# Performance work log

Measured on AMD Instinct MI355X. Metric: run time of the kernel, lower is better.

Reference implementation:

```python
import jax, jax.numpy as jnp
import numpy as np

N, C_IN, HF, WF = 4, 256, 128, 128
IMG_H, IMG_W = 1024, 1024
A = 3  # anchors per location (1 size x 3 aspect ratios), matches RPNHead
OBJ_THR, IOU_THR = 0.3, 0.7
PRE_NMS, POST_NMS = 2000, 300  # pre-NMS top-k (== top_k_proposals_training), post-NMS top-k (testing)


def setup_inputs() -> dict:
    key = jax.random.key(0)
    ks = jax.random.split(key, 5)
    return {
        "feat": jax.random.normal(ks[0], (N, C_IN, HF, WF), jnp.float32),
        "conv_w": jax.random.normal(ks[1], (256, C_IN, 3, 3), jnp.float32) * 0.02,
        "conv_b": jnp.zeros((256,), jnp.float32),
        "det_w": jax.random.normal(ks[2], (A, 256, 1, 1), jnp.float32) * 0.05,
        "det_b": jnp.zeros((A,), jnp.float32),
        "reg_w": jax.random.normal(ks[3], (4 * A, 256, 1, 1), jnp.float32) * 0.02,
        "reg_b": jnp.zeros((4 * A,), jnp.float32),
    }


def _conv(x, w, b, pad):
    y = jax.lax.conv_general_dilated(x, w, (1, 1), [(pad, pad), (pad, pad)],
                                     dimension_numbers=("NCHW", "OIHW", "NCHW"))
    return y + b[None, :, None, None]


def _anchors():
    # AnchorGenerator.generate_anchors + grid_anchors, stride = image // grid
    scales = jnp.array([128.0], jnp.float32)
    ratios = jnp.array([0.5, 1.0, 2.0], jnp.float32)
    hr = jnp.sqrt(ratios)
    wr = 1.0 / hr
    ws = (wr[:, None] * scales[None, :]).reshape(-1)
    hs = (hr[:, None] * scales[None, :]).reshape(-1)
    base = jnp.round(jnp.stack([-ws, -hs, ws, hs], axis=1) / 2.0)  # [A,4]
    sx = jnp.arange(WF, dtype=jnp.float32) * (IMG_W // WF)
    sy = jnp.arange(HF, dtype=jnp.float32) * (IMG_H // HF)
    yy, xx = jnp.meshgrid(sy, sx, indexing="ij")
    shifts = jnp.stack([xx.ravel(), yy.ravel(), xx.ravel(), yy.ravel()], axis=1)  # [H*W,4]
    return (shifts[:, None, :] + base[None, :, :]).reshape(-1, 4)  # [H*W*A,4]


def _decode(anchors, deltas):
    # Faithful to source, including the x/y swap in the anchor-center computation.
    x1, y1, x2, y2 = anchors[..., 0], anchors[..., 1], anchors[..., 2], anchors[..., 3]
    aw = x2 - x1
    ah = y2 - y1
    acx = y1 + aw / 2  # (sic) matches original code
    acy = x1 + ah / 2  # (sic)
    dx, dy, dw, dh = deltas[..., 0], deltas[..., 1], deltas[..., 2], deltas[..., 3]
    px = acx + dx * aw
    py = acy + dy * ah
    pw = aw * jnp.exp(dw)
    ph = ah * jnp.exp(dh)
    return jnp.stack([px - pw / 2, py - ph / 2, px + pw / 2, py + ph / 2], axis=-1)


def _filter_one(boxes, scores):
    # clip -> degenerate filter -> objectness threshold -> NMS -> top-k, fixed shapes
    w = boxes[:, 2] - boxes[:, 0]
    h = boxes[:, 3] - boxes[:, 1]
    valid = (scores > OBJ_THR) & (w > 0) & (h > 0)
    s = jnp.where(valid, scores, -jnp.inf)
    top_s, top_i = jax.lax.top_k(s, PRE_NMS)
    b = boxes[top_i]
    v = valid[top_i]
    area = jnp.maximum(b[:, 2] - b[:, 0], 0) * jnp.maximum(b[:, 3] - b[:, 1], 0)
    ix1 = jnp.maximum(b[:, None, 0], b[None, :, 0])
    iy1 = jnp.maximum(b[:, None, 1], b[None, :, 1])
    ix2 = jnp.minimum(b[:, None, 2], b[None, :, 2])
    iy2 = jnp.minimum(b[:, None, 3], b[None, :, 3])
    inter = jnp.maximum(ix2 - ix1, 0) * jnp.maximum(iy2 - iy1, 0)
    iou = inter / jnp.maximum(area[:, None] + area[None, :] - inter, 1e-9)
    idxs = jnp.arange(PRE_NMS)

    def body(keep, i):
        sup = jnp.any((iou[i] > IOU_THR) & keep & (idxs < i))
        return keep.at[i].set(v[i] & ~sup), None

    keep, _ = jax.lax.scan(body, jnp.zeros(PRE_NMS, bool), idxs)
    fs = jnp.where(keep, top_s, -jnp.inf)
    sel_s, sel_i = jax.lax.top_k(fs, POST_NMS)
    kept = keep[sel_i]
    out = jnp.concatenate([b[sel_i], sel_s[:, None]], axis=-1)  # [POST,5] = box + score
    return jnp.where(kept[:, None], out, 0.0)


def reference(feat, conv_w, conv_b, det_w, det_b, reg_w, reg_b):
    x = _conv(feat, conv_w, conv_b, 1)                      # fpn conv 3x3, no activation
    obj = jax.nn.sigmoid(_conv(x, det_w, det_b, 0)).reshape(N, -1)  # [N, A*H*W]
    d = _conv(x, reg_w, reg_b, 0)                           # [N, 4A, H, W]
    d = d.reshape(N, 4, A, HF, WF).transpose(0, 2, 3, 4, 1).reshape(N, -1, 4)
    anchors = _anchors()                                    # [A_total, 4]
    props = _decode(anchors[None], d)
    props = jnp.stack([
        jnp.clip(props[..., 0], 0, IMG_W), jnp.clip(props[..., 1], 0, IMG_H),
        jnp.clip(props[..., 2], 0, IMG_W), jnp.clip(props[..., 3], 0, IMG_H)], axis=-1)
    return jax.vmap(_filter_one)(props, obj)  # [N, POST_NMS, 5]
```

## Files before the change

### kernel.cpp

```cpp
#include <hip/hip_runtime.h>
#include <hip/hip_bf16.h>
#include <hip/hip_fp16.h>
#include <stdint.h>
#include <math.h>

#define N_IMG 4
#define CIN 256
#define HFD 128
#define WFD 128
#define HW (HFD*WFD)
#define NA 3
#define NPROP (NA*HW)
#define PRE_NMS 2000
#define POST_NMS 300

__device__ __forceinline__ unsigned long long rl64(unsigned long long v, int i) {
    unsigned int lo = (unsigned int)__builtin_amdgcn_readlane((int)(unsigned int)v, i);
    unsigned int hi = (unsigned int)__builtin_amdgcn_readlane((int)(unsigned int)(v >> 32), i);
    return ((unsigned long long)hi << 32) | (unsigned long long)lo;
}

__device__ __forceinline__ double sum8(const double* __restrict__ PART, size_t cp) {
    const size_t S = (size_t)1 << 20;
    double a = PART[cp] + PART[cp + S];
    double b = PART[cp + 2 * S] + PART[cp + 3 * S];
    double c = PART[cp + 4 * S] + PART[cp + 5 * S];
    double d = PART[cp + 6 * S] + PART[cp + 7 * S];
    return (a + b) + (c + d);
}

__device__ __forceinline__ void decode_box(int i, double dx, double dy, double dwv, double dhv,
                                           double& c1o, double& c2o, double& c3o, double& c4o) {
    int loc = i / 3, aa = i % 3;
    int hh = loc >> 7, wwi = loc & 127;
    double sx = (double)(wwi * 8), sy = (double)(hh * 8);
    double bx1 = (aa == 0) ? -91.0 : (aa == 1 ? -64.0 : -45.0);
    double by1 = (aa == 0) ? -45.0 : (aa == 1 ? -64.0 : -91.0);
    double x1 = sx + bx1, y1 = sy + by1, x2 = sx - bx1, y2 = sy - by1;
    double aw = x2 - x1, ahh = y2 - y1;
    double acx = y1 + aw * 0.5;
    double acy = x1 + ahh * 0.5;
    double px = acx + dx * aw, py = acy + dy * ahh;
    double pw = aw * exp(dwv), ph = ahh * exp(dhv);
    double c1 = px - pw * 0.5, c2 = py - ph * 0.5, c3 = px + pw * 0.5, c4 = py + ph * 0.5;
    c1o = fmin(fmax(c1, 0.0), 1024.0);
    c2o = fmin(fmax(c2, 0.0), 1024.0);
    c3o = fmin(fmax(c3, 0.0), 1024.0);
    c4o = fmin(fmax(c4, 0.0), 1024.0);
}

__global__ __launch_bounds__(256) void k_effw64(const float* __restrict__ cw, const float* __restrict__ cb,
                                                const float* __restrict__ dw_, const float* __restrict__ db_,
                                                const float* __restrict__ rw_, const float* __restrict__ rb_,
                                                double* __restrict__ E64, double* __restrict__ EB64)
{
    int b = blockIdx.x;
    int tid = threadIdx.x;
    if (b < 144) {
        __shared__ float hwl[15][260];
        __shared__ float wt[256][16];
        int k0 = b * 16;
        for (int idx = tid; idx < 15 * 256; idx += 256) {
            int c = idx >> 8, co = idx & 255;
            hwl[c][co] = (c < 3) ? dw_[c * 256 + co] : rw_[(c - 3) * 256 + co];
        }
        for (int idx = tid; idx < 4096; idx += 256) {
            int co = idx >> 4, kk = idx & 15;
            wt[co][kk] = cw[co * 2304 + k0 + kk];
        }
        __syncthreads();
        int kk = tid >> 4, c = tid & 15;
        double s = 0.0;
        if (c < 15) {
#pragma unroll 4
            for (int co = 0; co < 256; co++) s += (double)hwl[c][co] * (double)wt[co][kk];
        }
        E64[(k0 + kk) * 16 + c] = s;
    } else {
        if (tid < 16) {
            int c = tid;
            double s = 0.0; double hb = 0.0;
            if (c < 15) {
                const float* hw = (c < 3) ? (dw_ + c * 256) : (rw_ + (c - 3) * 256);
                for (int co = 0; co < 256; co++) s += (double)hw[co] * (double)cb[co];
                hb = (double)((c < 3) ? db_[c] : rb_[c - 3]);
            }
            EB64[c] = s + hb;
        }
    }
}

__global__ __launch_bounds__(256, 4) void k_conv64(const float* __restrict__ feat,
                                                   const double* __restrict__ E64,
                                                   double* __restrict__ PART)
{
    __shared__ float in_t[8][6][132];
    __shared__ double wl[8][9][16];
    int b = blockIdx.x;
    int chunk = b & 7; int htile = (b >> 3) & 31; int n = b >> 8;
    int h0 = htile * 4;
    int tid = threadIdx.x;
    int q = tid & 63, hl = tid >> 6;
    int w0 = q * 2;
    double acc[15][2];
#pragma unroll
    for (int c = 0; c < 15; c++) { acc[c][0] = 0.0; acc[c][1] = 0.0; }

    for (int sl = 0; sl < 4; sl++) {
        int ci0 = (chunk << 5) + sl * 8;
        for (int idx = tid; idx < 8 * 780; idx += 256) {
            int ci = idx / 780; int r2 = idx % 780; int dh = r2 / 130; int dw = r2 % 130;
            int gh = h0 - 1 + dh, gw = dw - 1;
            float v = 0.f;
            if (gh >= 0 && gh < HFD && gw >= 0 && gw < WFD)
                v = feat[(((n << 8) + ci0 + ci) << 14) + (gh << 7) + gw];
            in_t[ci][dh][dw] = v;
        }
        for (int idx = tid; idx < 1152; idx += 256) {
            ((double*)wl)[idx] = E64[(size_t)ci0 * 144 + idx];
        }
        __syncthreads();
        for (int ci = 0; ci < 8; ci++) {
#pragma unroll
            for (int r = 0; r < 3; r++) {
                float2 g0 = *(const float2*)&in_t[ci][hl + r][w0];
                float2 g1 = *(const float2*)&in_t[ci][hl + r][w0 + 2];
                float f[4] = {g0.x, g0.y, g1.x, g1.y};
#pragma unroll
                for (int s = 0; s < 3; s++) {
                    const double* wp = &wl[ci][r * 3 + s][0];
                    double pa = (double)f[s], pb = (double)f[s + 1];
#pragma unroll
                    for (int cp = 0; cp < 7; cp++) {
                        double2 wv = *(const double2*)(wp + 2 * cp);
                        acc[2 * cp][0] += wv.x * pa; acc[2 * cp][1] += wv.x * pb;
                        acc[2 * cp + 1][0] += wv.y * pa; acc[2 * cp + 1][1] += wv.y * pb;
                    }
                    double w14 = wp[14];
                    acc[14][0] += w14 * pa; acc[14][1] += w14 * pb;
                }
            }
        }
        __syncthreads();
    }
    int gpos = (n << 14) + ((h0 + hl) << 7) + w0;
    double* base = PART + ((size_t)chunk << 20) + gpos;
#pragma unroll
    for (int c = 0; c < 15; c++) {
        double2 st; st.x = acc[c][0]; st.y = acc[c][1];
        *(double2*)(base + (size_t)c * 65536) = st;
    }
}

__global__ __launch_bounds__(256) void k_findecode(const double* __restrict__ PART,
                                                   const double* __restrict__ EB64,
                                                   unsigned long long* __restrict__ KEY64)
{
    int p = blockIdx.x * 256 + threadIdx.x;
    int n = p >> 14, pos = p & 16383;
    double L[15];
#pragma unroll
    for (int c = 0; c < 15; c++)
        L[c] = sum8(PART, (size_t)c * 65536 + p) + EB64[c];
#pragma unroll
    for (int a = 0; a < 3; a++) {
        double logit = L[a];
        double score = 1.0 / (1.0 + exp(-logit));
        int i = a * HW + pos;
        double c1, c2, c3, c4;
        decode_box(i, L[3 + a], L[6 + a], L[9 + a], L[12 + a], c1, c2, c3, c4);
        bool valid = (score > 0.3) && (c3 - c1 > 0.0) && (c4 - c2 > 0.0);
        KEY64[(size_t)n * NPROP + i] = valid ? ~((unsigned long long)__double_as_longlong(score)) : ~0ull;
    }
}

__global__ __launch_bounds__(256) void k_selinit(unsigned long long* __restrict__ PSPREF,
                                                 int* __restrict__ PSNEED,
                                                 uint32_t* __restrict__ HIST,
                                                 uint32_t* __restrict__ CNT)
{
    int idx = blockIdx.x * 256 + threadIdx.x;
    if (idx < N_IMG * 2048) HIST[idx] = 0u;
    if (idx < N_IMG) { PSPREF[idx] = 0ull; PSNEED[idx] = PRE_NMS; CNT[idx] = 0u; }
}

__global__ __launch_bounds__(256) void k_hist(const unsigned long long* __restrict__ KEY64,
                                              const unsigned long long* __restrict__ PSPREF,
                                              uint32_t* __restrict__ HIST, int L)
{
    __shared__ uint32_t h[2048];
    int blk = blockIdx.x; int n = blk >> 4, sub = blk & 15;
    int tid = threadIdx.x;
    for (int i = tid; i < 2048; i += 256) h[i] = 0u;
    __syncthreads();
    int sh = 53 - 11 * L;
    unsigned long long pref = PSPREF[n];
    const unsigned long long* K = KEY64 + (size_t)n * NPROP + sub * 3072;
    for (int i = tid; i < 3072; i += 256) {
        unsigned long long k = K[i];
        bool in = (L == 0) || ((k >> (sh + 11)) == pref);
        if (in) atomicAdd(&h[(uint32_t)((k >> sh) & 2047ull)], 1u);
    }
    __syncthreads();
    uint32_t* G = HIST + n * 2048;
    for (int i = tid; i < 2048; i += 256) {
        uint32_t v = h[i];
        if (v) atomicAdd(&G[i], v);
    }
}

__global__ __launch_bounds__(256) void k_pick(uint32_t* __restrict__ HIST,
                                              unsigned long long* __restrict__ PSPREF,
                                              int* __restrict__ PSNEED)
{
    int n = blockIdx.x; int tid = threadIdx.x;
    __shared__ uint32_t hl[2048];
    __shared__ uint32_t psum[256];
    uint32_t* G = HIST + n * 2048;
    for (int i = tid; i < 2048; i += 256) hl[i] = G[i];
    __syncthreads();
    {
        uint32_t s = 0;
        for (int qq = 0; qq < 8; qq++) s += hl[tid * 8 + qq];
        psum[tid] = s;
    }
    __syncthreads();
    if (tid == 0) {
        int need = PSNEED[n];
        unsigned long long pref = PSPREF[n];
        uint32_t cum = 0; int g = 255;
        for (int t = 0; t < 256; t++) { uint32_t c = psum[t]; if (cum + c >= (uint32_t)need) { g = t; break; } cum += c; }
        int bsel = g * 8 + 7;
        for (int t = g * 8; t < g * 8 + 8; t++) { uint32_t c = hl[t]; if (cum + c >= (uint32_t)need) { bsel = t; break; } cum += c; }
        PSNEED[n] = need - (int)cum;
        PSPREF[n] = (pref << 11) | (unsigned long long)bsel;
    }
    __syncthreads();
    for (int i = tid; i < 2048; i += 256) G[i] = 0u;
}

__global__ __launch_bounds__(256) void k_collect(const unsigned long long* __restrict__ KEY64,
                                                 const unsigned long long* __restrict__ PSPREF,
                                                 uint32_t* __restrict__ CNT,
                                                 unsigned long long* __restrict__ CANDK,
                                                 uint32_t* __restrict__ CANDI)
{
    int blk = blockIdx.x; int n = blk >> 4, sub = blk & 15;
    int tid = threadIdx.x;
    unsigned long long pref44 = PSPREF[n];
    const unsigned long long* K = KEY64 + (size_t)n * NPROP;
    int base = sub * 3072;
    for (int i = tid; i < 3072; i += 256) {
        unsigned long long k = K[base + i];
        if (k != ~0ull && (k >> 20) <= pref44) {
            uint32_t p2 = atomicAdd(&CNT[n], 1u);
            if (p2 < 2048u) { CANDK[n * 2048 + p2] = k; CANDI[n * 2048 + p2] = (uint32_t)(base + i); }
        }
    }
}

__global__ __launch_bounds__(1024) void k_finalsel(const uint32_t* __restrict__ CNT,
                                                   const unsigned long long* __restrict__ CANDK,
                                                   const uint32_t* __restrict__ CANDI,
                                                   const double* __restrict__ PART,
                                                   const double* __restrict__ EB64,
                                                   unsigned long long* __restrict__ skeys,
                                                   double* __restrict__ bsort,
                                                   double* __restrict__ area)
{
    int n = blockIdx.x; int tid = threadIdx.x;
    __shared__ unsigned long long selk[2048];
    __shared__ uint32_t seli[2048];
    uint32_t cnt = CNT[n]; if (cnt > 2048u) cnt = 2048u;
    for (int t = tid; t < 2048; t += 1024) {
        if (t < (int)cnt) { selk[t] = CANDK[n * 2048 + t]; seli[t] = CANDI[n * 2048 + t]; }
        else { selk[t] = ~0ull; seli[t] = 0xFFFFFFFFu; }
    }
    __syncthreads();
    for (unsigned k2 = 2; k2 <= 2048; k2 <<= 1) {
        for (unsigned jx = k2 >> 1; jx > 0; jx >>= 1) {
            for (int t = tid; t < 2048; t += 1024) {
                unsigned ixj = (unsigned)t ^ jx;
                if (ixj > (unsigned)t) {
                    bool up = ((t & k2) == 0);
                    unsigned long long ka = selk[t], kb = selk[ixj];
                    uint32_t ia = seli[t], ib = seli[ixj];
                    bool agt = (ka > kb) || (ka == kb && ia > ib);
                    if (up ? agt : !agt) {
                        selk[t] = kb; selk[ixj] = ka;
                        seli[t] = ib; seli[ixj] = ia;
                    }
                }
            }
            __syncthreads();
        }
    }
    for (int t = tid; t < 2048; t += 1024) {
        bool valid = (t < PRE_NMS) && (selk[t] != ~0ull);
        if (t < PRE_NMS) skeys[(size_t)n * PRE_NMS + t] = valid ? selk[t] : ~0ull;
        double b0 = 0, b1 = 0, b2 = 0, b3 = 0;
        if (valid) {
            int i = (int)seli[t];
            int a = i >> 14, pos = i & 16383;
            size_t p = ((size_t)n << 14) + pos;
            double dx  = sum8(PART, (size_t)(3 + a)  * 65536 + p) + EB64[3 + a];
            double dy  = sum8(PART, (size_t)(6 + a)  * 65536 + p) + EB64[6 + a];
            double dwv = sum8(PART, (size_t)(9 + a)  * 65536 + p) + EB64[9 + a];
            double dhv = sum8(PART, (size_t)(12 + a) * 65536 + p) + EB64[12 + a];
            decode_box(i, dx, dy, dwv, dhv, b0, b1, b2, b3);
        }
        double* bs = bsort + (((size_t)(n * 2048 + t)) << 2);
        bs[0] = b0; bs[1] = b1; bs[2] = b2; bs[3] = b3;
        area[(size_t)n * 2048 + t] = fmax(b2 - b0, 0.0) * fmax(b3 - b1, 0.0);
    }
}

__global__ __launch_bounds__(256) void k_iou2(const double* __restrict__ bsort,
                                              const double* __restrict__ area,
                                              unsigned long long* __restrict__ mat)
{
    int blk = blockIdx.x; int n = blk >> 6; int rt = blk & 63;
    int tid = threadIdx.x;
    int r = tid >> 3, g = tid & 7;
    int i = rt * 32 + r;
    const double* bp = bsort + ((size_t)n * 2048 + i) * 4;
    double bx0 = bp[0], bx1_ = bp[1], bx2_ = bp[2], bx3 = bp[3];
    double ai = area[(size_t)n * 2048 + i];
    __shared__ double cbx[512][4];
    __shared__ double ca[512];
    for (int cc = 0; cc < 4; cc++) {
        if ((cc + 1) * 512 <= rt * 32) continue;
        __syncthreads();
        for (int idx = tid; idx < 512; idx += 256) {
            const double* sp = bsort + ((size_t)n * 2048 + cc * 512 + idx) * 4;
            cbx[idx][0] = sp[0]; cbx[idx][1] = sp[1]; cbx[idx][2] = sp[2]; cbx[idx][3] = sp[3];
            ca[idx] = area[(size_t)n * 2048 + cc * 512 + idx];
        }
        __syncthreads();
        unsigned long long wd = 0ull;
        for (int jb = 0; jb < 64; jb++) {
            int jr = (jb + g * 9) & 63;
            int jj = g * 64 + jr;
            double ix1 = fmax(bx0, cbx[jj][0]);
            double iy1 = fmax(bx1_, cbx[jj][1]);
            double ix2 = fmin(bx2_, cbx[jj][2]);
            double iy2 = fmin(bx3, cbx[jj][3]);
            double inter = fmax(ix2 - ix1, 0.0) * fmax(iy2 - iy1, 0.0);
            double den = fmax(ai + ca[jj] - inter, 1e-9);
            double iou = inter / den;
            if (iou > 0.7) wd |= (1ull << jr);
        }
        mat[((size_t)n * 2048 + i) * 32 + cc * 8 + g] = wd;
    }
}

__global__ __launch_bounds__(256) void k_nms3(const unsigned long long* __restrict__ skeys,
                                              const double* __restrict__ bsort,
                                              const unsigned long long* __restrict__ mat,
                                              float* __restrict__ out)
{
    int n = blockIdx.x; int tid = threadIdx.x;
    int lane = tid & 63;
    __shared__ unsigned long long rb[2][64][33];
    __shared__ unsigned long long sup_lds[32];
    __shared__ unsigned long long vb[32];
    __shared__ unsigned long long kbw[32];
    __shared__ int s_stop;
    float* dout = out + n * (POST_NMS * 5);
    for (int t = tid; t < POST_NMS * 5; t += 256) dout[t] = 0.f;
    if (tid < 32) { sup_lds[tid] = 0ull; kbw[tid] = 0ull; }
    if (tid == 0) s_stop = 0;
    if (tid < 64) {
        for (int i0 = 0; i0 < 2048; i0 += 64) {
            int i = i0 + lane;
            unsigned long long k = (i < PRE_NMS) ? skeys[(size_t)n * PRE_NMS + i] : ~0ull;
            unsigned long long m = __ballot(k != ~0ull);
            if (lane == 0) vb[i0 >> 6] = m;
        }
    }
    int r = tid >> 2, w0 = (tid & 3) * 8;
    {
        const unsigned long long* src = mat + ((size_t)n * 2048 + r) * 32 + w0;
        ulonglong2 a = *(const ulonglong2*)(src);
        ulonglong2 b = *(const ulonglong2*)(src + 2);
        ulonglong2 c2 = *(const ulonglong2*)(src + 4);
        ulonglong2 d = *(const ulonglong2*)(src + 6);
        unsigned long long* dst = &rb[0][r][w0];
        dst[0] = a.x; dst[1] = a.y; dst[2] = b.x; dst[3] = b.y;
        dst[4] = c2.x; dst[5] = c2.y; dst[6] = d.x; dst[7] = d.y;
    }
    __syncthreads();
    int total_kept = 0;
    for (int c = 0; c < 32; c++) {
        if (s_stop) break;
        int cur = c & 1, nxt = cur ^ 1;
        ulonglong2 pa, pb, pc, pd;
        bool pf = (c + 1 < 32);
        if (pf) {
            const unsigned long long* src = mat + ((size_t)n * 2048 + (c + 1) * 64 + r) * 32 + w0;
            pa = *(const ulonglong2*)(src);
            pb = *(const ulonglong2*)(src + 2);
            pc = *(const ulonglong2*)(src + 4);
            pd = *(const ulonglong2*)(src + 6);
        }
        if (tid < 64) {
            unsigned long long M = rb[cur][lane][c];
            unsigned long long supw = sup_lds[c];
            unsigned long long vbw = vb[c];
            unsigned long long km = 0ull;
#pragma unroll
            for (int ii = 0; ii < 64; ii++) {
                unsigned long long bit = 1ull << ii;
                if ((vbw & bit) && !(supw & bit)) {
                    km |= bit;
                    supw |= rl64(M, ii);
                }
            }
            if (lane == 0) {
                kbw[c] = km;
                total_kept += __popcll(km);
                if (total_kept >= POST_NMS) s_stop = 1;
            }
        }
        __syncthreads();
        {
            int w = tid & 31, g = tid >> 5;
            unsigned long long km2 = kbw[c];
            unsigned long long sub = (km2 >> (g * 8)) & 0xFFull;
            unsigned long long acc = 0ull;
            while (sub) {
                int bpos = __ffsll((long long)sub) - 1;
                sub &= sub - 1;
                acc |= rb[cur][g * 8 + bpos][w];
            }
            if (acc) atomicOr(&sup_lds[w], acc);
        }
        if (pf) {
            unsigned long long* dst = &rb[nxt][r][w0];
            dst[0] = pa.x; dst[1] = pa.y; dst[2] = pb.x; dst[3] = pb.y;
            dst[4] = pc.x; dst[5] = pc.y; dst[6] = pd.x; dst[7] = pd.y;
        }
        __syncthreads();
    }
    if (tid < 64) {
        int running = 0;
        for (int i0 = 0; i0 < 2048; i0 += 64) {
            int i = i0 + lane;
            bool kp = (i < PRE_NMS) && ((kbw[i >> 6] >> (i & 63)) & 1ull);
            unsigned long long m = __ballot(kp);
            if (kp) {
                int rk = running + __popcll(m & ((1ull << lane) - 1ull));
                if (rk < POST_NMS) {
                    const double* bp2 = bsort + ((size_t)n * 2048 + i) * 4;
                    unsigned long long k = skeys[(size_t)n * PRE_NMS + i];
                    double s = __longlong_as_double((long long)~k);
                    float* o = dout + rk * 5;
                    o[0] = (float)bp2[0]; o[1] = (float)bp2[1];
                    o[2] = (float)bp2[2]; o[3] = (float)bp2[3];
                    o[4] = (float)s;
                }
            }
            running += __popcll(m);
        }
    }
}

extern "C" void kernel_launch(void* const* d_in, const int* in_sizes, int n_in,
                              void* d_out, int out_size, void* d_ws, size_t ws_size,
                              hipStream_t stream) {
    (void)in_sizes; (void)n_in; (void)out_size; (void)ws_size;
    const float* feat   = (const float*)d_in[0];
    const float* conv_w = (const float*)d_in[1];
    const float* conv_b = (const float*)d_in[2];
    const float* det_w  = (const float*)d_in[3];
    const float* det_b  = (const float*)d_in[4];
    const float* reg_w  = (const float*)d_in[5];
    const float* reg_b  = (const float*)d_in[6];
    float* out = (float*)d_out;

    char* w = (char*)d_ws;
    double* E64 = (double*)w;                          w += (size_t)2304 * 16 * 8;
    double* EB64 = (double*)w;                         w += 128;
    double* PART = (double*)w;                         w += (size_t)8 << 23;
    unsigned long long* KEY64 = (unsigned long long*)w; w += (size_t)N_IMG * NPROP * 8;
    unsigned long long* PSPREF = (unsigned long long*)w; w += N_IMG * 8;
    int* PSNEED = (int*)w;                             w += 64;
    uint32_t* HIST = (uint32_t*)w;                     w += (size_t)N_IMG * 2048 * 4;
    uint32_t* CNT = (uint32_t*)w;                      w += 64;
    unsigned long long* CANDK = (unsigned long long*)w; w += (size_t)N_IMG * 2048 * 8;
    uint32_t* CANDI = (uint32_t*)w;                    w += (size_t)N_IMG * 2048 * 4;
    unsigned long long* SKEY = (unsigned long long*)w; w += (size_t)N_IMG * PRE_NMS * 8;
    double* BSORT = (double*)w;                        w += (size_t)N_IMG * 2048 * 4 * 8;
    double* AREA = (double*)w;                         w += (size_t)N_IMG * 2048 * 8;
    unsigned long long* MAT = (unsigned long long*)w;  w += (size_t)N_IMG * 2048 * 32 * 8;

    k_effw64<<<dim3(145), dim3(256), 0, stream>>>(conv_w, conv_b, det_w, det_b, reg_w, reg_b, E64, EB64);
    k_conv64<<<dim3(1024), dim3(256), 0, stream>>>(feat, E64, PART);
    k_findecode<<<dim3(256), dim3(256), 0, stream>>>(PART, EB64, KEY64);
    k_selinit<<<dim3(32), dim3(256), 0, stream>>>(PSPREF, PSNEED, HIST, CNT);
    for (int L = 0; L < 4; L++) {
        k_hist<<<dim3(64), dim3(256), 0, stream>>>(KEY64, PSPREF, HIST, L);
        k_pick<<<dim3(N_IMG), dim3(256), 0, stream>>>(HIST, PSPREF, PSNEED);
    }
    k_collect<<<dim3(64), dim3(256), 0, stream>>>(KEY64, PSPREF, CNT, CANDK, CANDI);
    k_finalsel<<<dim3(N_IMG), dim3(1024), 0, stream>>>(CNT, CANDK, CANDI, PART, EB64, SKEY, BSORT, AREA);
    k_iou2<<<dim3(N_IMG * 64), dim3(256), 0, stream>>>(BSORT, AREA, MAT);
    k_nms3<<<dim3(N_IMG), dim3(256), 0, stream>>>(SKEY, BSORT, MAT, out);
}
```

Before: 444.8 us.

## Repartition conv work across output channels and fuse first histogram pass into decode

The folded conv kernel now gives each block one output row and 64 input channels across 4 chunks, with each thread group computing 4 of the 15 output channels instead of all 15. This cuts the per-thread accumulator registers, allowing higher occupancy (launch bounds 7), and halves the partial-sum buffer traffic. The first radix-select histogram level is built in k_findecode with shared-memory atomics, and the init kernel is merged into k_effw64, removing two launches and one full pass over the keys. In exchange, the input tile is reloaded per row, with more halo overhead relative to useful work.

```diff
diff --git a/kernel.cpp b/kernel.cpp
--- a/kernel.cpp
+++ b/kernel.cpp
@@ -20,13 +20,9 @@
     return ((unsigned long long)hi << 32) | (unsigned long long)lo;
 }
 
-__device__ __forceinline__ double sum8(const double* __restrict__ PART, size_t cp) {
+__device__ __forceinline__ double sum4(const double* __restrict__ PART, size_t cp) {
     const size_t S = (size_t)1 << 20;
-    double a = PART[cp] + PART[cp + S];
-    double b = PART[cp + 2 * S] + PART[cp + 3 * S];
-    double c = PART[cp + 4 * S] + PART[cp + 5 * S];
-    double d = PART[cp + 6 * S] + PART[cp + 7 * S];
-    return (a + b) + (c + d);
+    return (PART[cp] + PART[cp + S]) + (PART[cp + 2 * S] + PART[cp + 3 * S]);
 }
 
 __device__ __forceinline__ void decode_box(int i, double dx, double dy, double dwv, double dhv,
@@ -52,7 +48,11 @@
 __global__ __launch_bounds__(256) void k_effw64(const float* __restrict__ cw, const float* __restrict__ cb,
                                                 const float* __restrict__ dw_, const float* __restrict__ db_,
                                                 const float* __restrict__ rw_, const float* __restrict__ rb_,
-                                                double* __restrict__ E64, double* __restrict__ EB64)
+                                                double* __restrict__ E64, double* __restrict__ EB64,
+                                                unsigned long long* __restrict__ PSPREF,
+                                                int* __restrict__ PSNEED,
+                                                uint32_t* __restrict__ HIST,
+                                                uint32_t* __restrict__ CNT)
 {
     int b = blockIdx.x;
     int tid = threadIdx.x;
@@ -87,34 +87,35 @@
             }
             EB64[c] = s + hb;
         }
-    }
-}
-
-__global__ __launch_bounds__(256, 4) void k_conv64(const float* __restrict__ feat,
+        for (int i = tid; i < N_IMG * 2048; i += 256) HIST[i] = 0u;
+        if (tid < N_IMG) { PSPREF[tid] = 0ull; PSNEED[tid] = PRE_NMS; CNT[tid] = 0u; }
+    }
+}
+
+__global__ __launch_bounds__(256, 7) void k_conv64(const float* __restrict__ feat,
                                                    const double* __restrict__ E64,
                                                    double* __restrict__ PART)
 {
-    __shared__ float in_t[8][6][132];
+    __shared__ float in_t[8][3][132];
     __shared__ double wl[8][9][16];
     int b = blockIdx.x;
-    int chunk = b & 7; int htile = (b >> 3) & 31; int n = b >> 8;
-    int h0 = htile * 4;
+    int chunk = b & 3; int h = (b >> 2) & 127; int n = b >> 9;
     int tid = threadIdx.x;
-    int q = tid & 63, hl = tid >> 6;
+    int q = tid & 63, g = tid >> 6;
     int w0 = q * 2;
-    double acc[15][2];
-#pragma unroll
-    for (int c = 0; c < 15; c++) { acc[c][0] = 0.0; acc[c][1] = 0.0; }
-
-    for (int sl = 0; sl < 4; sl++) {
-        int ci0 = (chunk << 5) + sl * 8;
-        for (int idx = tid; idx < 8 * 780; idx += 256) {
-            int ci = idx / 780; int r2 = idx % 780; int dh = r2 / 130; int dw = r2 % 130;
-            int gh = h0 - 1 + dh, gw = dw - 1;
+    double acc[4][2];
+#pragma unroll
+    for (int cc = 0; cc < 4; cc++) { acc[cc][0] = 0.0; acc[cc][1] = 0.0; }
+
+    for (int sl = 0; sl < 8; sl++) {
+        int ci0 = (chunk << 6) + sl * 8;
+        for (int idx = tid; idx < 8 * 396; idx += 256) {
+            int ci = idx / 396; int rem = idx % 396; int dr = rem / 132; int dw = rem % 132;
+            int gh = h - 1 + dr, gw = dw - 1;
             float v = 0.f;
             if (gh >= 0 && gh < HFD && gw >= 0 && gw < WFD)
                 v = feat[(((n << 8) + ci0 + ci) << 14) + (gh << 7) + gw];
-            in_t[ci][dh][dw] = v;
+            in_t[ci][dr][dw] = v;
         }
         for (int idx = tid; idx < 1152; idx += 256) {
             ((double*)wl)[idx] = E64[(size_t)ci0 * 144 + idx];
@@ -123,45 +124,51 @@
         for (int ci = 0; ci < 8; ci++) {
 #pragma unroll
             for (int r = 0; r < 3; r++) {
-                float2 g0 = *(const float2*)&in_t[ci][hl + r][w0];
-                float2 g1 = *(const float2*)&in_t[ci][hl + r][w0 + 2];
+                float2 g0 = *(const float2*)&in_t[ci][r][w0];
+                float2 g1 = *(const float2*)&in_t[ci][r][w0 + 2];
                 float f[4] = {g0.x, g0.y, g1.x, g1.y};
 #pragma unroll
                 for (int s = 0; s < 3; s++) {
-                    const double* wp = &wl[ci][r * 3 + s][0];
+                    const double* wp = &wl[ci][r * 3 + s][g * 4];
+                    double2 wv0 = *(const double2*)(wp);
+                    double2 wv1 = *(const double2*)(wp + 2);
                     double pa = (double)f[s], pb = (double)f[s + 1];
-#pragma unroll
-                    for (int cp = 0; cp < 7; cp++) {
-                        double2 wv = *(const double2*)(wp + 2 * cp);
-                        acc[2 * cp][0] += wv.x * pa; acc[2 * cp][1] += wv.x * pb;
-                        acc[2 * cp + 1][0] += wv.y * pa; acc[2 * cp + 1][1] += wv.y * pb;
-                    }
-                    double w14 = wp[14];
-                    acc[14][0] += w14 * pa; acc[14][1] += w14 * pb;
+                    acc[0][0] += wv0.x * pa; acc[0][1] += wv0.x * pb;
+                    acc[1][0] += wv0.y * pa; acc[1][1] += wv0.y * pb;
+                    acc[2][0] += wv1.x * pa; acc[2][1] += wv1.x * pb;
+                    acc[3][0] += wv1.y * pa; acc[3][1] += wv1.y * pb;
                 }
             }
         }
         __syncthreads();
     }
-    int gpos = (n << 14) + ((h0 + hl) << 7) + w0;
+    int gpos = (n << 14) + (h << 7) + w0;
     double* base = PART + ((size_t)chunk << 20) + gpos;
 #pragma unroll
-    for (int c = 0; c < 15; c++) {
-        double2 st; st.x = acc[c][0]; st.y = acc[c][1];
-        *(double2*)(base + (size_t)c * 65536) = st;
+    for (int cc = 0; cc < 4; cc++) {
+        int c = g * 4 + cc;
+        if (c < 15) {
+            double2 st; st.x = acc[cc][0]; st.y = acc[cc][1];
+            *(double2*)(base + (size_t)c * 65536) = st;
+        }
     }
 }
 
 __global__ __launch_bounds__(256) void k_findecode(const double* __restrict__ PART,
                                                    const double* __restrict__ EB64,
-                                                   unsigned long long* __restrict__ KEY64)
-{
-    int p = blockIdx.x * 256 + threadIdx.x;
+                                                   unsigned long long* __restrict__ KEY64,
+                                                   uint32_t* __restrict__ HIST)
+{
+    __shared__ uint32_t h2[2048];
+    int tid = threadIdx.x;
+    for (int i = tid; i < 2048; i += 256) h2[i] = 0u;
+    __syncthreads();
+    int p = blockIdx.x * 256 + tid;
     int n = p >> 14, pos = p & 16383;
     double L[15];
 #pragma unroll
     for (int c = 0; c < 15; c++)
-        L[c] = sum8(PART, (size_t)c * 65536 + p) + EB64[c];
+        L[c] = sum4(PART, (size_t)c * 65536 + p) + EB64[c];
 #pragma unroll
     for (int a = 0; a < 3; a++) {
         double logit = L[a];
@@ -170,18 +177,16 @@
         double c1, c2, c3, c4;
         decode_box(i, L[3 + a], L[6 + a], L[9 + a], L[12 + a], c1, c2, c3, c4);
         bool valid = (score > 0.3) && (c3 - c1 > 0.0) && (c4 - c2 > 0.0);
-        KEY64[(size_t)n * NPROP + i] = valid ? ~((unsigned long long)__double_as_longlong(score)) : ~0ull;
-    }
-}
-
-__global__ __launch_bounds__(256) void k_selinit(unsigned long long* __restrict__ PSPREF,
-                                                 int* __restrict__ PSNEED,
-                                                 uint32_t* __restrict__ HIST,
-                                                 uint32_t* __restrict__ CNT)
-{
-    int idx = blockIdx.x * 256 + threadIdx.x;
-    if (idx < N_IMG * 2048) HIST[idx] = 0u;
-    if (idx < N_IMG) { PSPREF[idx] = 0ull; PSNEED[idx] = PRE_NMS; CNT[idx] = 0u; }
+        unsigned long long key = valid ? ~((unsigned long long)__double_as_longlong(score)) : ~0ull;
+        KEY64[(size_t)n * NPROP + i] = key;
+        atomicAdd(&h2[(uint32_t)(key >> 53)], 1u);
+    }
+    __syncthreads();
+    uint32_t* G = HIST + n * 2048;
+    for (int i = tid; i < 2048; i += 256) {
+        uint32_t v = h2[i];
+        if (v) atomicAdd(&G[i], v);
+    }
 }
 
 __global__ __launch_bounds__(256) void k_hist(const unsigned long long* __restrict__ KEY64,
@@ -303,10 +308,10 @@
             int i = (int)seli[t];
             int a = i >> 14, pos = i & 16383;
             size_t p = ((size_t)n << 14) + pos;
-            double dx  = sum8(PART, (size_t)(3 + a)  * 65536 + p) + EB64[3 + a];
-            double dy  = sum8(PART, (size_t)(6 + a)  * 65536 + p) + EB64[6 + a];
-            double dwv = sum8(PART, (size_t)(9 + a)  * 65536 + p) + EB64[9 + a];
-            double dhv = sum8(PART, (size_t)(12 + a) * 65536 + p) + EB64[12 + a];
+            double dx  = sum4(PART, (size_t)(3 + a)  * 65536 + p) + EB64[3 + a];
+            double dy  = sum4(PART, (size_t)(6 + a)  * 65536 + p) + EB64[6 + a];
+            double dwv = sum4(PART, (size_t)(9 + a)  * 65536 + p) + EB64[9 + a];
+            double dhv = sum4(PART, (size_t)(12 + a) * 65536 + p) + EB64[12 + a];
             decode_box(i, dx, dy, dwv, dhv, b0, b1, b2, b3);
         }
         double* bs = bsort + (((size_t)(n * 2048 + t)) << 2);
@@ -481,7 +486,7 @@
     char* w = (char*)d_ws;
     double* E64 = (double*)w;                          w += (size_t)2304 * 16 * 8;
     double* EB64 = (double*)w;                         w += 128;
-    double* PART = (double*)w;                         w += (size_t)8 << 23;
+    double* PART = (double*)w;                         w += (size_t)4 << 23;
     unsigned long long* KEY64 = (unsigned long long*)w; w += (size_t)N_IMG * NPROP * 8;
     unsigned long long* PSPREF = (unsigned long long*)w; w += N_IMG * 8;
     int* PSNEED = (int*)w;                             w += 64;
@@ -494,11 +499,12 @@
     double* AREA = (double*)w;                         w += (size_t)N_IMG * 2048 * 8;
     unsigned long long* MAT = (unsigned long long*)w;  w += (size_t)N_IMG * 2048 * 32 * 8;
 
-    k_effw64<<<dim3(145), dim3(256), 0, stream>>>(conv_w, conv_b, det_w, det_b, reg_w, reg_b, E64, EB64);
-    k_conv64<<<dim3(1024), dim3(256), 0, stream>>>(feat, E64, PART);
-    k_findecode<<<dim3(256), dim3(256), 0, stream>>>(PART, EB64, KEY64);
-    k_selinit<<<dim3(32), dim3(256), 0, stream>>>(PSPREF, PSNEED, HIST, CNT);
-    for (int L = 0; L < 4; L++) {
+    k_effw64<<<dim3(145), dim3(256), 0, stream>>>(conv_w, conv_b, det_w, det_b, reg_w, reg_b,
+                                                  E64, EB64, PSPREF, PSNEED, HIST, CNT);
+    k_conv64<<<dim3(2048), dim3(256), 0, stream>>>(feat, E64, PART);
+    k_findecode<<<dim3(256), dim3(256), 0, stream>>>(PART, EB64, KEY64, HIST);
+    k_pick<<<dim3(N_IMG), dim3(256), 0, stream>>>(HIST, PSPREF, PSNEED);
+    for (int L = 1; L < 4; L++) {
         k_hist<<<dim3(64), dim3(256), 0, stream>>>(KEY64, PSPREF, HIST, L);
         k_pick<<<dim3(N_IMG), dim3(256), 0, stream>>>(HIST, PSPREF, PSNEED);
     }
```

Measured after the change: 416.6 us. 6.3% less time.
